# Performance work log

Hardware: AMD Instinct MI355X
Metric: run time of the kernel (lower is better)

Reference implementation:

```python
import jax, jax.numpy as jnp
import numpy as np

N = 200000      # active voxels
F_IN = 64
F_OUT = 128
K = 27          # 3x3x3 kernel offsets
EPS = 1e-5


def setup_inputs() -> dict:
    key = jax.random.key(0)
    ks = jax.random.split(key, 7)
    x = jax.random.normal(ks[0], (N, F_IN), dtype=jnp.float32)
    gamma = jax.random.uniform(ks[1], (F_IN,), dtype=jnp.float32, minval=0.5, maxval=1.5)
    beta = jax.random.normal(ks[2], (F_IN,), dtype=jnp.float32) * 0.1
    running_mean = jax.random.normal(ks[3], (F_IN,), dtype=jnp.float32) * 0.1
    running_var = jax.random.uniform(ks[4], (F_IN,), dtype=jnp.float32, minval=0.5, maxval=1.5)
    W = jax.random.normal(ks[5], (K, F_IN, F_OUT), dtype=jnp.float32) * (1.0 / np.sqrt(K * F_IN))
    # Precomputed kernel-offset neighbor map (hash-table lookups in torchsparse).
    neighbor_idx = jax.random.randint(ks[6], (N, K), 0, N, dtype=jnp.int32)
    # Submanifold conv: center offset (k=13) always maps a voxel to itself.
    neighbor_idx = neighbor_idx.at[:, K // 2].set(jnp.arange(N, dtype=jnp.int32))
    return {"x": x, "gamma": gamma, "beta": beta, "running_mean": running_mean,
            "running_var": running_var, "W": W, "neighbor_idx": neighbor_idx}


def reference(x, gamma, beta, running_mean, running_var, W, neighbor_idx):
    # BatchNorm (inference, per-feature affine) + SiLU, fused elementwise.
    scale = gamma * jax.lax.rsqrt(running_var + EPS)          # [F_in]
    y = jax.nn.silu((x - running_mean) * scale + beta)        # [N, F_in]
    # Submanifold sparse conv as gather + implicit GEMM over K offsets.
    g = y[neighbor_idx]                                       # [N, K, F_in]
    out = jnp.einsum('nkf,kfo->no', g, W)                     # [N, F_out]
    return out
```

## Files before the change

### kernel.cpp

```cpp
#include <hip/hip_runtime.h>
#include <cstdint>
#include <cstddef>


typedef __attribute__((ext_vector_type(8))) short short8;
typedef __attribute__((ext_vector_type(4))) float f32x4;

#define N_VOX 200000
#define F_IN 64
#define F_OUT 128
#define KOFF 27
#define BM 128

__device__ __forceinline__ short f2bf(float f) {
  unsigned u = __builtin_bit_cast(unsigned, f);
  u += 0x7fffu + ((u >> 16) & 1u);
  return (short)(u >> 16);
}

__global__ __launch_bounds__(256) void bn_silu_kernel(
    const float* __restrict__ x, const float* __restrict__ gamma,
    const float* __restrict__ beta, const float* __restrict__ mean,
    const float* __restrict__ var, short* __restrict__ y) {
  __shared__ float s_scale[F_IN], s_bias[F_IN];
  int tid = threadIdx.x;
  if (tid < F_IN) {
    float s = gamma[tid] * rsqrtf(var[tid] + 1e-5f);
    s_scale[tid] = s;
    s_bias[tid] = beta[tid] - mean[tid] * s;
  }
  __syncthreads();
  size_t i = ((size_t)blockIdx.x * 256 + tid) * 8;
  int f0 = (int)(i & (F_IN - 1));
  float4 x0 = *(const float4*)(x + i);
  float4 x1 = *(const float4*)(x + i + 4);
  float v[8] = {x0.x, x0.y, x0.z, x0.w, x1.x, x1.y, x1.z, x1.w};
  short8 o;
#pragma unroll
  for (int j = 0; j < 8; ++j) {
    float t = v[j] * s_scale[f0 + j] + s_bias[f0 + j];
    float sg = 1.0f / (1.0f + __expf(-t));
    o[j] = f2bf(t * sg);
  }
  *(short8*)(y + i) = o;
}

__global__ __launch_bounds__(256) void wprep_kernel(
    const float* __restrict__ W, short* __restrict__ Wt) {
  int tid = blockIdx.x * 256 + threadIdx.x;
  if (tid >= KOFF * F_OUT * 8) return;
  int k = tid >> 10;
  int r = tid & 1023;
  int o = r >> 3;
  int f0 = (r & 7) * 8;
  short8 vv;
#pragma unroll
  for (int i = 0; i < 8; ++i)
    vv[i] = f2bf(W[((size_t)k * F_IN + f0 + i) * F_OUT + o]);
  *(short8*)(Wt + ((size_t)k * F_OUT + o) * F_IN + f0) = vv;
}


__global__ __launch_bounds__(512, 4) void conv_mfma_kernel(
    const short* __restrict__ y,
    const short* __restrict__ Wt,
    const int* __restrict__ nidx,
    float* __restrict__ out) {
  __shared__ __align__(16) short Atile[2][BM * F_IN];

  const int tid = threadIdx.x;
  const int wave = tid >> 6;
  const int lane = tid & 63;
  const int lhi = lane >> 4;
  const int llo = lane & 15;
  const int row0 = blockIdx.x * BM;

  const int m0 = wave * 16 + (lane >> 3);
  const int m1 = m0 + 8;
  const int c = lane & 7;
  const int wr0 = m0 * 128 + ((c ^ (m0 & 7)) << 4);
  const int wr1 = wr0 + 1024;
  const int gr0 = (row0 + m0 < N_VOX) ? row0 + m0 : N_VOX - 1;
  const int gr1 = (row0 + m1 < N_VOX) ? row0 + m1 : N_VOX - 1;
  const int* ip0 = nidx + (size_t)gr0 * KOFF;
  const int* ip1 = nidx + (size_t)gr1 * KOFF;
  const short* wtp = Wt + (size_t)(wave * 16 + llo) * F_IN + lhi * 8;

  f32x4 acc[8] = {};
  short8 b0[2], b1[2];
  short8 arA0, arA1, arB0, arB1;

  {
    const int g0 = ip0[0], g1 = ip1[0];
    short8 t0 = *(const short8*)(y + (size_t)g0 * F_IN + c * 8);
    short8 t1 = *(const short8*)(y + (size_t)g1 * F_IN + c * 8);
    const int h0 = ip0[1], h1 = ip1[1];
    arA0 = *(const short8*)(y + (size_t)h0 * F_IN + c * 8);
    arA1 = *(const short8*)(y + (size_t)h1 * F_IN + c * 8);
    b0[0] = *(const short8*)(wtp);
    b0[1] = *(const short8*)(wtp + 32);
    *(short8*)((char*)Atile[0] + wr0) = t0;
    *(short8*)((char*)Atile[0] + wr1) = t1;
  }
  __syncthreads();

#define CONV_BODY(K, BUF, BCUR, BNEXT, AC0, AC1, AN0, AN1)                     \
  {                                                                            \
    if ((K) + 2 < KOFF) {                                                      \
      const int g0 = ip0[(K) + 2], g1 = ip1[(K) + 2];                          \
      AN0 = *(const short8*)(y + (size_t)g0 * F_IN + c * 8);                   \
      AN1 = *(const short8*)(y + (size_t)g1 * F_IN + c * 8);                   \
    }                                                                          \
    if ((K) + 1 < KOFF) {                                                      \
      (BNEXT)[0] = *(const short8*)(wtp + (size_t)((K) + 1) * 8192);           \
      (BNEXT)[1] = *(const short8*)(wtp + (size_t)((K) + 1) * 8192 + 32);      \
    }                                                                          \
    __builtin_amdgcn_sched_barrier(0);     \
    _Pragma("unroll")                                                          \
    for (int rt = 0; rt < 8; ++rt) {                                           \
      const int mm = rt * 16 + llo;                                            \
      const int base = mm * 128 + lhi * 16;                                    \
      const int swz = (mm & 7) << 4;                                           \
      short8 a0 = *(const short8*)((const char*)Atile[BUF] + (base ^ swz));    \
      short8 a1 =                                                              \
          *(const short8*)((const char*)Atile[BUF] + ((base + 64) ^ swz));     \
      acc[rt] = __builtin_amdgcn_mfma_f32_16x16x32_bf16(a0, (BCUR)[0],         \
                                                        acc[rt], 0, 0, 0);     \
      acc[rt] = __builtin_amdgcn_mfma_f32_16x16x32_bf16(a1, (BCUR)[1],         \
                                                        acc[rt], 0, 0, 0);     \
    }                                                                          \
    __builtin_amdgcn_sched_barrier(0);         \
    if ((K) + 1 < KOFF) {                                                      \
      *(short8*)((char*)Atile[(BUF) ^ 1] + wr0) = AC0;                         \
      *(short8*)((char*)Atile[(BUF) ^ 1] + wr1) = AC1;                         \
    }                                                                          \
    __syncthreads();                                                           \
  }

  for (int k = 0; k < KOFF - 1; k += 2) {
    CONV_BODY(k, 0, b0, b1, arA0, arA1, arB0, arB1);
    CONV_BODY(k + 1, 1, b1, b0, arB0, arB1, arA0, arA1);
  }
  CONV_BODY(KOFF - 1, 0, b0, b1, arA0, arA1, arB0, arB1);
#undef CONV_BODY

#pragma unroll
  for (int rt = 0; rt < 8; ++rt) {
    const int col = wave * 16 + llo;
    const int rbase = row0 + rt * 16 + lhi * 4;
#pragma unroll
    for (int j = 0; j < 4; ++j) {
      const int row = rbase + j;
      if (row < N_VOX) out[(size_t)row * F_OUT + col] = acc[rt][j];
    }
  }
}

extern "C" void kernel_launch(void* const* d_in, const int* in_sizes, int n_in,
                              void* d_out, int out_size, void* d_ws, size_t ws_size,
                              hipStream_t stream) {
  const float* x     = (const float*)d_in[0];
  const float* gamma = (const float*)d_in[1];
  const float* beta  = (const float*)d_in[2];
  const float* rmean = (const float*)d_in[3];
  const float* rvar  = (const float*)d_in[4];
  const float* W     = (const float*)d_in[5];
  const int*   nidx  = (const int*)d_in[6];
  float* out = (float*)d_out;

  short* y_bf16  = (short*)d_ws;
  short* Wt_bf16 = (short*)((char*)d_ws + (size_t)N_VOX * F_IN * 2);

  bn_silu_kernel<<<(N_VOX * F_IN) / (256 * 8), 256, 0, stream>>>(
      x, gamma, beta, rmean, rvar, y_bf16);

  wprep_kernel<<<(KOFF * F_OUT * 8 + 255) / 256, 256, 0, stream>>>(W, Wt_bf16);

  conv_mfma_kernel<<<(N_VOX + BM - 1) / BM, 512, 0, stream>>>(
      y_bf16, Wt_bf16, nidx, out);
}
```

Measured before the change: 179.9 us.

## Shrink conv tile to 64 rows with 2x2 wave grid and deferred gather

```diff
diff --git a/kernel.cpp b/kernel.cpp
--- a/kernel.cpp
+++ b/kernel.cpp
@@ -10,7 +10,7 @@
 #define F_IN 64
 #define F_OUT 128
 #define KOFF 27
-#define BM 128
+#define BM 64
 
 __device__ __forceinline__ short f2bf(float f) {
   unsigned u = __builtin_bit_cast(unsigned, f);
@@ -61,7 +61,7 @@
 }
 
 
-__global__ __launch_bounds__(512, 4) void conv_mfma_kernel(
+__global__ __launch_bounds__(256, 4) void conv_mfma_kernel(
     const short* __restrict__ y,
     const short* __restrict__ Wt,
     const int* __restrict__ nidx,
@@ -73,6 +73,8 @@
   const int lane = tid & 63;
   const int lhi = lane >> 4;
   const int llo = lane & 15;
+  const int rg = wave >> 1;
+  const int cg = wave & 1;
   const int row0 = blockIdx.x * BM;
 
   const int m0 = wave * 16 + (lane >> 3);
@@ -80,80 +82,89 @@
   const int c = lane & 7;
   const int wr0 = m0 * 128 + ((c ^ (m0 & 7)) << 4);
   const int wr1 = wr0 + 1024;
-  const int gr0 = (row0 + m0 < N_VOX) ? row0 + m0 : N_VOX - 1;
-  const int gr1 = (row0 + m1 < N_VOX) ? row0 + m1 : N_VOX - 1;
-  const int* ip0 = nidx + (size_t)gr0 * KOFF;
-  const int* ip1 = nidx + (size_t)gr1 * KOFF;
-  const short* wtp = Wt + (size_t)(wave * 16 + llo) * F_IN + lhi * 8;
+  const int* ip0 = nidx + (size_t)(row0 + m0) * KOFF;
+  const int* ip1 = nidx + (size_t)(row0 + m1) * KOFF;
+  const short* wtp = Wt + (size_t)(cg * 64 + llo) * F_IN + lhi * 8;
 
-  f32x4 acc[8] = {};
-  short8 b0[2], b1[2];
-  short8 arA0, arA1, arB0, arB1;
+  f32x4 acc[2][4] = {};
+  short8 bA[4][2], bB[4][2];
+  int i_a0, i_a1, i_b0, i_b1;
 
   {
     const int g0 = ip0[0], g1 = ip1[0];
     short8 t0 = *(const short8*)(y + (size_t)g0 * F_IN + c * 8);
     short8 t1 = *(const short8*)(y + (size_t)g1 * F_IN + c * 8);
-    const int h0 = ip0[1], h1 = ip1[1];
-    arA0 = *(const short8*)(y + (size_t)h0 * F_IN + c * 8);
-    arA1 = *(const short8*)(y + (size_t)h1 * F_IN + c * 8);
-    b0[0] = *(const short8*)(wtp);
-    b0[1] = *(const short8*)(wtp + 32);
+    i_a0 = ip0[1];
+    i_a1 = ip1[1];
+#pragma unroll
+    for (int ct = 0; ct < 4; ++ct)
+#pragma unroll
+      for (int kh = 0; kh < 2; ++kh)
+        bA[ct][kh] = *(const short8*)(wtp + ct * 1024 + kh * 32);
     *(short8*)((char*)Atile[0] + wr0) = t0;
     *(short8*)((char*)Atile[0] + wr1) = t1;
   }
   __syncthreads();
 
-#define CONV_BODY(K, BUF, BCUR, BNEXT, AC0, AC1, AN0, AN1)                     \
+#define CONV_BODY(K, BUF, BCUR, BNEXT, IC0, IC1, IN0, IN1)                     \
   {                                                                            \
+    short8 as0, as1;                                                           \
     if ((K) + 2 < KOFF) {                                                      \
-      const int g0 = ip0[(K) + 2], g1 = ip1[(K) + 2];                          \
-      AN0 = *(const short8*)(y + (size_t)g0 * F_IN + c * 8);                   \
-      AN1 = *(const short8*)(y + (size_t)g1 * F_IN + c * 8);                   \
+      IN0 = ip0[(K) + 2];                                                      \
+      IN1 = ip1[(K) + 2];                                                      \
     }                                                                          \
     if ((K) + 1 < KOFF) {                                                      \
-      (BNEXT)[0] = *(const short8*)(wtp + (size_t)((K) + 1) * 8192);           \
-      (BNEXT)[1] = *(const short8*)(wtp + (size_t)((K) + 1) * 8192 + 32);      \
+      as0 = *(const short8*)(y + (size_t)IC0 * F_IN + c * 8);                  \
+      as1 = *(const short8*)(y + (size_t)IC1 * F_IN + c * 8);                  \
+      _Pragma("unroll")                                                        \
+      for (int ct = 0; ct < 4; ++ct)                                           \
+        _Pragma("unroll")                                                      \
+        for (int kh = 0; kh < 2; ++kh)                                         \
+          (BNEXT)[ct][kh] = *(const short8*)(wtp + (size_t)((K) + 1) * 8192 +  \
+                                             ct * 1024 + kh * 32);             \
     }                                                                          \
     __builtin_amdgcn_sched_barrier(0);     \
     _Pragma("unroll")                                                          \
-    for (int rt = 0; rt < 8; ++rt) {                                           \
-      const int mm = rt * 16 + llo;                                            \
+    for (int rt = 0; rt < 2; ++rt) {                                           \
+      const int mm = rg * 32 + rt * 16 + llo;                                  \
       const int base = mm * 128 + lhi * 16;                                    \
       const int swz = (mm & 7) << 4;                                           \
       short8 a0 = *(const short8*)((const char*)Atile[BUF] + (base ^ swz));    \
       short8 a1 =                                                              \
           *(const short8*)((const char*)Atile[BUF] + ((base + 64) ^ swz));     \
-      acc[rt] = __builtin_amdgcn_mfma_f32_16x16x32_bf16(a0, (BCUR)[0],         \
-                                                        acc[rt], 0, 0, 0);     \
-      acc[rt] = __builtin_amdgcn_mfma_f32_16x16x32_bf16(a1, (BCUR)[1],         \
-                                                        acc[rt], 0, 0, 0);     \
+      _Pragma("unroll")                                                        \
+      for (int ct = 0; ct < 4; ++ct) {                                         \
+        acc[rt][ct] = __builtin_amdgcn_mfma_f32_16x16x32_bf16(                 \
+            a0, (BCUR)[ct][0], acc[rt][ct], 0, 0, 0);                          \
+        acc[rt][ct] = __builtin_amdgcn_mfma_f32_16x16x32_bf16(                 \
+            a1, (BCUR)[ct][1], acc[rt][ct], 0, 0, 0);                          \
+      }                                                                        \
     }                                                                          \
     __builtin_amdgcn_sched_barrier(0);         \
     if ((K) + 1 < KOFF) {                                                      \
-      *(short8*)((char*)Atile[(BUF) ^ 1] + wr0) = AC0;                         \
-      *(short8*)((char*)Atile[(BUF) ^ 1] + wr1) = AC1;                         \
+      *(short8*)((char*)Atile[(BUF) ^ 1] + wr0) = as0;                         \
+      *(short8*)((char*)Atile[(BUF) ^ 1] + wr1) = as1;                         \
     }                                                                          \
     __syncthreads();                                                           \
   }
 
   for (int k = 0; k < KOFF - 1; k += 2) {
-    CONV_BODY(k, 0, b0, b1, arA0, arA1, arB0, arB1);
-    CONV_BODY(k + 1, 1, b1, b0, arB0, arB1, arA0, arA1);
+    CONV_BODY(k, 0, bA, bB, i_a0, i_a1, i_b0, i_b1);
+    CONV_BODY(k + 1, 1, bB, bA, i_b0, i_b1, i_a0, i_a1);
   }
-  CONV_BODY(KOFF - 1, 0, b0, b1, arA0, arA1, arB0, arB1);
+  CONV_BODY(KOFF - 1, 0, bA, bB, i_a0, i_a1, i_b0, i_b1);
 #undef CONV_BODY
 
 #pragma unroll
-  for (int rt = 0; rt < 8; ++rt) {
-    const int col = wave * 16 + llo;
-    const int rbase = row0 + rt * 16 + lhi * 4;
+  for (int rt = 0; rt < 2; ++rt)
 #pragma unroll
-    for (int j = 0; j < 4; ++j) {
-      const int row = rbase + j;
-      if (row < N_VOX) out[(size_t)row * F_OUT + col] = acc[rt][j];
+    for (int ct = 0; ct < 4; ++ct) {
+      const int col = cg * 64 + ct * 16 + llo;
+      const int rbase = row0 + rg * 32 + rt * 16 + lhi * 4;
+#pragma unroll
+      for (int j = 0; j < 4; ++j)
+        out[(size_t)(rbase + j) * F_OUT + col] = acc[rt][ct][j];
     }
-  }
 }
 
 extern "C" void kernel_launch(void* const* d_in, const int* in_sizes, int n_in,
@@ -176,6 +187,5 @@
 
   wprep_kernel<<<(KOFF * F_OUT * 8 + 255) / 256, 256, 0, stream>>>(W, Wt_bf16);
 
-  conv_mfma_kernel<<<(N_VOX + BM - 1) / BM, 512, 0, stream>>>(
-      y_bf16, Wt_bf16, nidx, out);
+  conv_mfma_kernel<<<N_VOX / BM, 256, 0, stream>>>(y_bf16, Wt_bf16, nidx, out);
 }
```

Measured after the change: 504.6 us. 2.8x slower.

## Process two kernel offsets per barrier with four-buffer LDS pipeline

Applied to the files above, without the earlier changes.

```diff
diff --git a/kernel.cpp b/kernel.cpp
--- a/kernel.cpp
+++ b/kernel.cpp
@@ -66,7 +66,7 @@
     const short* __restrict__ Wt,
     const int* __restrict__ nidx,
     float* __restrict__ out) {
-  __shared__ __align__(16) short Atile[2][BM * F_IN];
+  __shared__ __align__(16) short Atile[4][BM * F_IN];
 
   const int tid = threadIdx.x;
   const int wave = tid >> 6;
@@ -87,62 +87,92 @@
   const short* wtp = Wt + (size_t)(wave * 16 + llo) * F_IN + lhi * 8;
 
   f32x4 acc[8] = {};
-  short8 b0[2], b1[2];
-  short8 arA0, arA1, arB0, arB1;
+  short8 BPa[2][2], BPb[2][2];
+  int ia0, ia1, ib0, ib1;
+  int ja0, ja1, jb0, jb1;
 
   {
-    const int g0 = ip0[0], g1 = ip1[0];
+    const int g0 = ip0[0], g1 = ip1[0], h0 = ip0[1], h1 = ip1[1];
     short8 t0 = *(const short8*)(y + (size_t)g0 * F_IN + c * 8);
     short8 t1 = *(const short8*)(y + (size_t)g1 * F_IN + c * 8);
-    const int h0 = ip0[1], h1 = ip1[1];
-    arA0 = *(const short8*)(y + (size_t)h0 * F_IN + c * 8);
-    arA1 = *(const short8*)(y + (size_t)h1 * F_IN + c * 8);
-    b0[0] = *(const short8*)(wtp);
-    b0[1] = *(const short8*)(wtp + 32);
+    short8 t2 = *(const short8*)(y + (size_t)h0 * F_IN + c * 8);
+    short8 t3 = *(const short8*)(y + (size_t)h1 * F_IN + c * 8);
+    ia0 = ip0[2]; ia1 = ip1[2]; ja0 = ip0[3]; ja1 = ip1[3];
+#pragma unroll
+    for (int kt = 0; kt < 2; ++kt) {
+      BPa[0][kt] = *(const short8*)(wtp + kt * 32);
+      BPa[1][kt] = *(const short8*)(wtp + 8192 + kt * 32);
+    }
     *(short8*)((char*)Atile[0] + wr0) = t0;
     *(short8*)((char*)Atile[0] + wr1) = t1;
+    *(short8*)((char*)Atile[1] + wr0) = t2;
+    *(short8*)((char*)Atile[1] + wr1) = t3;
   }
   __syncthreads();
 
-#define CONV_BODY(K, BUF, BCUR, BNEXT, AC0, AC1, AN0, AN1)                     \
+#define MFMA_HALF(RB, BPK)                                                     \
+  _Pragma("unroll")                                                            \
+  for (int rt = 0; rt < 8; ++rt) {                                             \
+    const int mm = rt * 16 + llo;                                              \
+    const int base = mm * 128 + lhi * 16;                                      \
+    const int swz = (mm & 7) << 4;                                             \
+    short8 a0 = *(const short8*)((const char*)Atile[RB] + (base ^ swz));       \
+    short8 a1 = *(const short8*)((const char*)Atile[RB] + ((base + 64) ^ swz));\
+    acc[rt] = __builtin_amdgcn_mfma_f32_16x16x32_bf16(a0, (BPK)[0],            \
+                                                      acc[rt], 0, 0, 0);       \
+    acc[rt] = __builtin_amdgcn_mfma_f32_16x16x32_bf16(a1, (BPK)[1],            \
+                                                      acc[rt], 0, 0, 0);       \
+  }
+
+#define SUPER(K, R0, R1, W0, W1, BP, BQ, IC2_0, IC2_1, IC3_0, IC3_1,           \
+              IN4_0, IN4_1, IN5_0, IN5_1)                                      \
   {                                                                            \
+    short8 as0, as1, as2, as3;                                                 \
     if ((K) + 2 < KOFF) {                                                      \
-      const int g0 = ip0[(K) + 2], g1 = ip1[(K) + 2];                          \
-      AN0 = *(const short8*)(y + (size_t)g0 * F_IN + c * 8);                   \
-      AN1 = *(const short8*)(y + (size_t)g1 * F_IN + c * 8);                   \
-    }                                                                          \
-    if ((K) + 1 < KOFF) {                                                      \
-      (BNEXT)[0] = *(const short8*)(wtp + (size_t)((K) + 1) * 8192);           \
-      (BNEXT)[1] = *(const short8*)(wtp + (size_t)((K) + 1) * 8192 + 32);      \
-    }                                                                          \
-    __builtin_amdgcn_sched_barrier(0);     \
-    _Pragma("unroll")                                                          \
-    for (int rt = 0; rt < 8; ++rt) {                                           \
-      const int mm = rt * 16 + llo;                                            \
-      const int base = mm * 128 + lhi * 16;                                    \
-      const int swz = (mm & 7) << 4;                                           \
-      short8 a0 = *(const short8*)((const char*)Atile[BUF] + (base ^ swz));    \
-      short8 a1 =                                                              \
-          *(const short8*)((const char*)Atile[BUF] + ((base + 64) ^ swz));     \
-      acc[rt] = __builtin_amdgcn_mfma_f32_16x16x32_bf16(a0, (BCUR)[0],         \
-                                                        acc[rt], 0, 0, 0);     \
-      acc[rt] = __builtin_amdgcn_mfma_f32_16x16x32_bf16(a1, (BCUR)[1],         \
-                                                        acc[rt], 0, 0, 0);     \
-    }                                                                          \
+      as0 = *(const short8*)(y + (size_t)IC2_0 * F_IN + c * 8);                \
+      as1 = *(const short8*)(y + (size_t)IC2_1 * F_IN + c * 8);                \
+      _Pragma("unroll")                                                        \
+      for (int kt = 0; kt < 2; ++kt)                                           \
+        (BQ)[0][kt] =                                                          \
+            *(const short8*)(wtp + (size_t)((K) + 2) * 8192 + kt * 32);        \
+    }                                                                          \
+    if ((K) + 3 < KOFF) {                                                      \
+      as2 = *(const short8*)(y + (size_t)IC3_0 * F_IN + c * 8);                \
+      as3 = *(const short8*)(y + (size_t)IC3_1 * F_IN + c * 8);                \
+      _Pragma("unroll")                                                        \
+      for (int kt = 0; kt < 2; ++kt)                                           \
+        (BQ)[1][kt] =                                                          \
+            *(const short8*)(wtp + (size_t)((K) + 3) * 8192 + kt * 32);        \
+    }                                                                          \
+    if ((K) + 4 < KOFF) { IN4_0 = ip0[(K) + 4]; IN4_1 = ip1[(K) + 4]; }        \
+    if ((K) + 5 < KOFF) { IN5_0 = ip0[(K) + 5]; IN5_1 = ip1[(K) + 5]; }        \
+    __builtin_amdgcn_sched_barrier(0);    \
+    __builtin_amdgcn_s_setprio(1);                                             \
+    MFMA_HALF(R0, (BP)[0])                                                     \
+    MFMA_HALF(R1, (BP)[1])                                                     \
+    __builtin_amdgcn_s_setprio(0);                                             \
     __builtin_amdgcn_sched_barrier(0);         \
-    if ((K) + 1 < KOFF) {                                                      \
-      *(short8*)((char*)Atile[(BUF) ^ 1] + wr0) = AC0;                         \
-      *(short8*)((char*)Atile[(BUF) ^ 1] + wr1) = AC1;                         \
+    if ((K) + 2 < KOFF) {                                                      \
+      *(short8*)((char*)Atile[W0] + wr0) = as0;                                \
+      *(short8*)((char*)Atile[W0] + wr1) = as1;                                \
+    }                                                                          \
+    if ((K) + 3 < KOFF) {                                                      \
+      *(short8*)((char*)Atile[W1] + wr0) = as2;                                \
+      *(short8*)((char*)Atile[W1] + wr1) = as3;                                \
     }                                                                          \
     __syncthreads();                                                           \
   }
 
-  for (int k = 0; k < KOFF - 1; k += 2) {
-    CONV_BODY(k, 0, b0, b1, arA0, arA1, arB0, arB1);
-    CONV_BODY(k + 1, 1, b1, b0, arB0, arB1, arA0, arA1);
-  }
-  CONV_BODY(KOFF - 1, 0, b0, b1, arA0, arA1, arB0, arB1);
-#undef CONV_BODY
+  for (int k = 0; k < 24; k += 4) {
+    SUPER(k, 0, 1, 2, 3, BPa, BPb, ia0, ia1, ja0, ja1, ib0, ib1, jb0, jb1);
+    SUPER(k + 2, 2, 3, 0, 1, BPb, BPa, ib0, ib1, jb0, jb1, ia0, ia1, ja0, ja1);
+  }
+  SUPER(24, 0, 1, 2, 3, BPa, BPb, ia0, ia1, ja0, ja1, ib0, ib1, jb0, jb1);
+  __builtin_amdgcn_s_setprio(1);
+  MFMA_HALF(2, BPb[0])
+  __builtin_amdgcn_s_setprio(0);
+#undef SUPER
+#undef MFMA_HALF
 
 #pragma unroll
   for (int rt = 0; rt < 8; ++rt) {
```

Measured after the change: 217.2 us. +20.7%, slower.

## Deepen gather pipeline to three stages and lighten per-offset barriers

Applied to the files above, without the earlier changes.

```diff
diff --git a/kernel.cpp b/kernel.cpp
--- a/kernel.cpp
+++ b/kernel.cpp
@@ -87,62 +87,81 @@
   const short* wtp = Wt + (size_t)(wave * 16 + llo) * F_IN + lhi * 8;
 
   f32x4 acc[8] = {};
-  short8 b0[2], b1[2];
-  short8 arA0, arA1, arB0, arB1;
+  short8 s0a, s0b, s1a, s1b, s2a, s2b;
+  short8 BA[2], BB[2];
+  int iA0, iA1, iB0, iB1;
 
   {
     const int g0 = ip0[0], g1 = ip1[0];
-    short8 t0 = *(const short8*)(y + (size_t)g0 * F_IN + c * 8);
-    short8 t1 = *(const short8*)(y + (size_t)g1 * F_IN + c * 8);
     const int h0 = ip0[1], h1 = ip1[1];
-    arA0 = *(const short8*)(y + (size_t)h0 * F_IN + c * 8);
-    arA1 = *(const short8*)(y + (size_t)h1 * F_IN + c * 8);
-    b0[0] = *(const short8*)(wtp);
-    b0[1] = *(const short8*)(wtp + 32);
-    *(short8*)((char*)Atile[0] + wr0) = t0;
-    *(short8*)((char*)Atile[0] + wr1) = t1;
-  }
-  __syncthreads();
-
-#define CONV_BODY(K, BUF, BCUR, BNEXT, AC0, AC1, AN0, AN1)                     \
+    const int e0 = ip0[2], e1 = ip1[2];
+    s0a = *(const short8*)(y + (size_t)g0 * F_IN + c * 8);
+    s0b = *(const short8*)(y + (size_t)g1 * F_IN + c * 8);
+    s1a = *(const short8*)(y + (size_t)h0 * F_IN + c * 8);
+    s1b = *(const short8*)(y + (size_t)h1 * F_IN + c * 8);
+    s2a = *(const short8*)(y + (size_t)e0 * F_IN + c * 8);
+    s2b = *(const short8*)(y + (size_t)e1 * F_IN + c * 8);
+    iA0 = ip0[3]; iA1 = ip1[3];
+    BA[0] = *(const short8*)(wtp);
+    BA[1] = *(const short8*)(wtp + 32);
+    *(short8*)((char*)Atile[0] + wr0) = s0a;
+    *(short8*)((char*)Atile[0] + wr1) = s0b;
+  }
+  __builtin_amdgcn_sched_barrier(0);
+  asm volatile("s_waitcnt lgkmcnt(0)" ::: "memory");
+  __builtin_amdgcn_s_barrier();
+  __builtin_amdgcn_sched_barrier(0);
+
+#define PHASE(K, RBUF, SIa, SIb, SWa, SWb, BCUR, BNEXT, IUa, IUb, ILa, ILb)    \
   {                                                                            \
-    if ((K) + 2 < KOFF) {                                                      \
-      const int g0 = ip0[(K) + 2], g1 = ip1[(K) + 2];                          \
-      AN0 = *(const short8*)(y + (size_t)g0 * F_IN + c * 8);                   \
-      AN1 = *(const short8*)(y + (size_t)g1 * F_IN + c * 8);                   \
+    if ((K) + 3 < KOFF) {                                                      \
+      SIa = *(const short8*)(y + (size_t)(IUa) * F_IN + c * 8);                \
+      SIb = *(const short8*)(y + (size_t)(IUb) * F_IN + c * 8);                \
+    }                                                                          \
+    if ((K) + 4 < KOFF) {                                                      \
+      ILa = ip0[(K) + 4];                                                      \
+      ILb = ip1[(K) + 4];                                                      \
     }                                                                          \
     if ((K) + 1 < KOFF) {                                                      \
       (BNEXT)[0] = *(const short8*)(wtp + (size_t)((K) + 1) * 8192);           \
       (BNEXT)[1] = *(const short8*)(wtp + (size_t)((K) + 1) * 8192 + 32);      \
-    }                                                                          \
-    __builtin_amdgcn_sched_barrier(0);     \
+      *(short8*)((char*)Atile[(RBUF) ^ 1] + wr0) = SWa;                        \
+      *(short8*)((char*)Atile[(RBUF) ^ 1] + wr1) = SWb;                        \
+    }                                                                          \
+    __builtin_amdgcn_sched_barrier(0);                                         \
     _Pragma("unroll")                                                          \
     for (int rt = 0; rt < 8; ++rt) {                                           \
       const int mm = rt * 16 + llo;                                            \
       const int base = mm * 128 + lhi * 16;                                    \
       const int swz = (mm & 7) << 4;                                           \
-      short8 a0 = *(const short8*)((const char*)Atile[BUF] + (base ^ swz));    \
+      short8 a0 = *(const short8*)((const char*)Atile[RBUF] + (base ^ swz));   \
       short8 a1 =                                                              \
-          *(const short8*)((const char*)Atile[BUF] + ((base + 64) ^ swz));     \
+          *(const short8*)((const char*)Atile[RBUF] + ((base + 64) ^ swz));    \
       acc[rt] = __builtin_amdgcn_mfma_f32_16x16x32_bf16(a0, (BCUR)[0],         \
                                                         acc[rt], 0, 0, 0);     \
       acc[rt] = __builtin_amdgcn_mfma_f32_16x16x32_bf16(a1, (BCUR)[1],         \
                                                         acc[rt], 0, 0, 0);     \
     }                                                                          \
-    __builtin_amdgcn_sched_barrier(0);         \
+    __builtin_amdgcn_sched_barrier(0);                                         \
     if ((K) + 1 < KOFF) {                                                      \
-      *(short8*)((char*)Atile[(BUF) ^ 1] + wr0) = AC0;                         \
-      *(short8*)((char*)Atile[(BUF) ^ 1] + wr1) = AC1;                         \
-    }                                                                          \
-    __syncthreads();                                                           \
-  }
-
-  for (int k = 0; k < KOFF - 1; k += 2) {
-    CONV_BODY(k, 0, b0, b1, arA0, arA1, arB0, arB1);
-    CONV_BODY(k + 1, 1, b1, b0, arB0, arB1, arA0, arA1);
-  }
-  CONV_BODY(KOFF - 1, 0, b0, b1, arA0, arA1, arB0, arB1);
-#undef CONV_BODY
+      asm volatile("s_waitcnt lgkmcnt(0)" ::: "memory");                       \
+      __builtin_amdgcn_s_barrier();                                            \
+      __builtin_amdgcn_sched_barrier(0);                                       \
+    }                                                                          \
+  }
+
+  for (int k = 0; k < 24; k += 6) {
+    PHASE(k + 0, 0, s0a, s0b, s1a, s1b, BA, BB, iA0, iA1, iB0, iB1);
+    PHASE(k + 1, 1, s1a, s1b, s2a, s2b, BB, BA, iB0, iB1, iA0, iA1);
+    PHASE(k + 2, 0, s2a, s2b, s0a, s0b, BA, BB, iA0, iA1, iB0, iB1);
+    PHASE(k + 3, 1, s0a, s0b, s1a, s1b, BB, BA, iB0, iB1, iA0, iA1);
+    PHASE(k + 4, 0, s1a, s1b, s2a, s2b, BA, BB, iA0, iA1, iB0, iB1);
+    PHASE(k + 5, 1, s2a, s2b, s0a, s0b, BB, BA, iB0, iB1, iA0, iA1);
+  }
+  PHASE(24, 0, s0a, s0b, s1a, s1b, BA, BB, iA0, iA1, iB0, iB1);
+  PHASE(25, 1, s1a, s1b, s2a, s2b, BB, BA, iB0, iB1, iA0, iA1);
+  PHASE(26, 0, s2a, s2b, s0a, s0b, BA, BB, iA0, iA1, iB0, iB1);
+#undef PHASE
 
 #pragma unroll
   for (int rt = 0; rt < 8; ++rt) {
```

Result: no change. 180.8 us (+0.5%).
